# Kernel optimization log

Hardware: AMD Instinct MI355X
Metric: run time of the kernel (lower is better)

Reference implementation:

```python
import jax, jax.numpy as jnp
import numpy as np

N, E, G = 20000, 160000, 64
IN_FULL, X_START, X_END = 16, 4, 10
H, OUT, RH, NE, K = 512, 512, 128, 4, 2
NL = 3               # GraphConv layers per expert
SPS, STEMP = 0.3, 1.0  # size_prior_strength, size_temperature


def setup_inputs() -> dict:
    key = jax.random.key(0)
    ks = jax.random.split(key, 10)
    def w(k, shape, fan):
        return jax.random.normal(k, shape, jnp.float32) / np.float32(np.sqrt(fan))
    return dict(
        x=jax.random.normal(ks[0], (N, IN_FULL), jnp.float32),
        edge_index=jax.random.randint(ks[1], (2, E), 0, N),
        batch=jnp.sort(jax.random.randint(ks[2], (N,), 0, G)),
        num_graphs=G,
        enc_W1=w(ks[3], (X_END - X_START, H), X_END - X_START), enc_b1=jnp.zeros((H,), jnp.float32),
        enc_W2=w(ks[4], (H, H), H), enc_b2=jnp.zeros((H,), jnp.float32),
        r_W1=w(ks[5], (H + 2, RH), H + 2), r_b1=jnp.zeros((RH,), jnp.float32),
        ln_g=jnp.ones((RH,), jnp.float32), ln_b=jnp.zeros((RH,), jnp.float32),
        r_W2=w(ks[6], (RH, NE), RH), r_b2=jnp.zeros((NE,), jnp.float32),
        size_centers=jnp.linspace(0.0, 1.0, NE).astype(jnp.float32),
        W_rel=w(ks[7], (NE, NL, H, H), H),       # GraphConv lin_rel weights (stacked)
        b_rel=jnp.zeros((NE, NL, H), jnp.float32),
        W_root=w(ks[8], (NE, NL, H, H), H),      # GraphConv lin_root weights (no bias)
    )


def reference(x, edge_index, batch, num_graphs, enc_W1, enc_b1, enc_W2, enc_b2,
              r_W1, r_b1, ln_g, ln_b, r_W2, r_b2, size_centers, W_rel, b_rel, W_root):
    src, dst = edge_index[0], edge_index[1]
    # encoder: Linear -> ReLU -> Linear on sliced node features
    h = jax.nn.relu(x[:, X_START:X_END] @ enc_W1 + enc_b1) @ enc_W2 + enc_b2
    # per-graph size features (log_nodes_edges mode)
    nodes = jnp.maximum(jax.ops.segment_sum(jnp.ones((N,), x.dtype), batch, num_segments=num_graphs), 1.0)
    edges = jax.ops.segment_sum(jnp.ones((E,), x.dtype), batch[src], num_segments=num_graphs)
    log_n, log_e = jnp.log(nodes), jnp.log1p(edges)
    f = jnp.stack([log_n, log_e], axis=-1)
    f = (f - f.mean(0, keepdims=True)) / (f.std(0, keepdims=True) + 1e-6)
    size_norm = (log_n - log_n.min()) / (log_n.max() - log_n.min() + 1e-6)
    # router: Linear -> LayerNorm -> ReLU -> Linear, plus size prior
    r = jnp.concatenate([h, f[batch]], axis=-1) @ r_W1 + r_b1
    r = (r - r.mean(-1, keepdims=True)) / jnp.sqrt(r.var(-1, keepdims=True) + 1e-5) * ln_g + ln_b
    logits = jax.nn.relu(r) @ r_W2 + r_b2
    prior = -(size_norm[batch][:, None] - size_centers[None, :]) ** 2 / STEMP
    logits = (1.0 - SPS) * logits + SPS * prior
    probs = jax.nn.softmax(logits, axis=-1)
    # top-k sparse gating, renormalized
    v, ix = jax.lax.top_k(probs, K)
    v = v / (v.sum(-1, keepdims=True) + 1e-8)
    weights = jnp.zeros_like(probs).at[jnp.arange(N)[:, None], ix].set(v)  # [N, NE]
    # GraphConv: out_i = (sum_{j->i} z_j) @ W_rel + b_rel + z_i @ W_root
    def gconv(z, Wr, br, Wo):
        agg = jax.ops.segment_sum(z[src], dst, num_segments=N)
        return agg @ Wr + br + z @ Wo
    out = jnp.zeros((N, OUT), x.dtype)
    for e in range(NE):  # small fixed expert count
        z = jax.nn.relu(gconv(h, W_rel[e, 0], b_rel[e, 0], W_root[e, 0]))
        z = jax.nn.relu(gconv(z, W_rel[e, 1], b_rel[e, 1], W_root[e, 1]))
        z = gconv(z, W_rel[e, 2], b_rel[e, 2], W_root[e, 2])
        out = out + weights[:, e:e + 1] * z
    return out
```

## Files before the change

### kernel.cpp

```cpp
#include <hip/hip_runtime.h>
#include <math.h>

#define N_NODES 20000
#define N_EDGES 160000
#define G_GRAPHS 64
#define H_DIM 512
#define RH_DIM 128
#define NE_EXP 4
#define P_ROWS 20096
#define EH_BLOCKS 64
#define WSZ (512 * 512)

typedef __attribute__((ext_vector_type(8))) short bf16x8;
typedef __attribute__((ext_vector_type(4))) float f32x4;

__device__ __forceinline__ ushort f2bf(float f) {
    uint u = __float_as_uint(f);
    return (ushort)((u + 0x7FFFu + ((u >> 16) & 1u)) >> 16);
}
__device__ __forceinline__ float bf2f(ushort h) {
    return __uint_as_float(((uint)h) << 16);
}

__device__ __forceinline__ void async_copy16(const void* g, void* l) {
    __builtin_amdgcn_global_load_lds(
        (__attribute__((address_space(1))) void*)g,
        (__attribute__((address_space(3))) void*)l, 16, 0, 0);
}

__device__ __forceinline__ int xcd_swizzle(int orig, int nwg) {
    const int q = nwg >> 3, r = nwg & 7;
    const int xcd = orig & 7, sid = orig >> 3;
    return (xcd < r ? xcd * (q + 1) : r * (q + 1) + (xcd - r) * q) + sid;
}

template<bool RELU, int EPI, int NE2>
__global__ __launch_bounds__(256)
void gemm_grp(const ushort* __restrict__ A1, size_t a1es,
              const ushort* __restrict__ W1, size_t w1es,
              const ushort* __restrict__ A2, size_t a2es,
              const ushort* __restrict__ W2, size_t w2es,
              const float* __restrict__ bias, size_t bes,
              const float* __restrict__ wcol,
              ushort* __restrict__ out0, size_t oes)
{
    __shared__ char smem[32768];
    const int tid = threadIdx.x;
    const int w = tid >> 6, lane = tid & 63;

    const int wgid = xcd_swizzle(blockIdx.x, gridDim.x);
    const int m0 = (wgid / (4 * NE2)) * 128;
    const int rem = wgid % (4 * NE2);
    const int e  = rem % NE2;
    const int n0 = (rem / NE2) * 128;

    const ushort* __restrict__ A1e = A1 + (size_t)e * a1es;
    const ushort* __restrict__ W1e = W1 + (size_t)e * w1es;
    const ushort* __restrict__ A2e = A2 + (size_t)e * a2es;
    const ushort* __restrict__ W2e = W2 + (size_t)e * w2es;
    const float*  __restrict__ be  = bias + (size_t)e * bes;
    ushort* __restrict__ oe = out0 + (size_t)e * oes;

    f32x4 acc[4][4];
#pragma unroll
    for (int i = 0; i < 4; ++i)
#pragma unroll
        for (int j = 0; j < 4; ++j) acc[i][j] = (f32x4){0.f, 0.f, 0.f, 0.f};

    const int srow = lane >> 2, schk = lane & 3;
    const int wr = w >> 1, wc = w & 1;
    const int row16 = lane & 15;
    const uint koffB = (uint)(lane >> 4) * 16u;
    const uint aoff0 = (uint)(wr * 64 + row16) * 64u + koffB;
    const uint boff0 = 8192u + (uint)(wc * 64 + row16) * 64u + koffB;

    auto stage = [&](int buf, int t) {
        const ushort* __restrict__ A  = (t < 16) ? A1e : A2e;
        const ushort* __restrict__ Wt = (t < 16) ? W1e : W2e;
        const int kt = (t & 15) * 32;
        char* base = smem + buf * 16384;
#pragma unroll
        for (int c = 0; c < 2; ++c) {
            const int rb = c * 64 + w * 16;
            async_copy16(A  + (size_t)(m0 + rb + srow) * 512 + kt + schk * 8, base + rb * 64);
            async_copy16(Wt + (size_t)(n0 + rb + srow) * 512 + kt + schk * 8, base + 8192 + rb * 64);
        }
    };
    auto compute = [&](int buf) {
        const char* base = smem + buf * 16384;
        bf16x8 af[4], bfr[4];
#pragma unroll
        for (int i = 0; i < 4; ++i) af[i] = *(const bf16x8*)(base + aoff0 + i * 1024);
#pragma unroll
        for (int j = 0; j < 4; ++j) bfr[j] = *(const bf16x8*)(base + boff0 + j * 1024);
#pragma unroll
        for (int i = 0; i < 4; ++i)
#pragma unroll
            for (int j = 0; j < 4; ++j)
                acc[i][j] = __builtin_amdgcn_mfma_f32_16x16x32_bf16(af[i], bfr[j], acc[i][j], 0, 0, 0);
    };

    stage(0, 0);
    for (int t = 0; t < 31; ++t) {
        stage((t + 1) & 1, t + 1);
        asm volatile("s_waitcnt vmcnt(4)" ::: "memory");
        __builtin_amdgcn_s_barrier();
        compute(t & 1);
        __builtin_amdgcn_s_barrier();
    }
    asm volatile("s_waitcnt vmcnt(0)" ::: "memory");
    __builtin_amdgcn_s_barrier();
    compute(1);

#pragma unroll
    for (int i = 0; i < 4; ++i) {
        const int r0 = m0 + wr * 64 + i * 16 + (lane >> 4) * 4;
#pragma unroll
        for (int j = 0; j < 4; ++j) {
            const int c = n0 + wc * 64 + j * 16 + row16;
            const float bj = be[c];
#pragma unroll
            for (int q2 = 0; q2 < 4; ++q2) {
                const int r = r0 + q2;
                float v = acc[i][j][q2] + bj;
                if (EPI == 0) {
                    if (RELU) v = fmaxf(v, 0.f);
                    oe[(size_t)r * 512 + c] = f2bf(v);
                } else {
                    const float wrow = (r < N_NODES) ? wcol[(size_t)r * 4 + e] : 0.f;
                    oe[(size_t)r * 512 + c] = f2bf(v * wrow);
                }
            }
        }
    }
}

template<int NPASS, int EPI, int NBN>
__global__ __launch_bounds__(256)
void gemm_mfma(const ushort* __restrict__ A0, const ushort* __restrict__ W0,
               const ushort* __restrict__ A1p, const ushort* __restrict__ W1p,
               const ushort* __restrict__ A2p, const ushort* __restrict__ W2p,
               const float* __restrict__ bias,
               void* __restrict__ out0, void* __restrict__ out1, int Ncols)
{
    __shared__ char smem[32768];
    const int tid = threadIdx.x;
    const int w = tid >> 6, lane = tid & 63;

    const int wgid = xcd_swizzle(blockIdx.x, gridDim.x);
    const int m0 = (wgid / NBN) * 128;
    const int n0 = (wgid % NBN) * 128;

    f32x4 acc[4][4];
#pragma unroll
    for (int i = 0; i < 4; ++i)
#pragma unroll
        for (int j = 0; j < 4; ++j) acc[i][j] = (f32x4){0.f, 0.f, 0.f, 0.f};

    const int srow = lane >> 2, schk = lane & 3;
    const int wr = w >> 1, wc = w & 1;
    const int row16 = lane & 15;
    const uint koffB = (uint)(lane >> 4) * 16u;
    const uint aoff0 = (uint)(wr * 64 + row16) * 64u + koffB;
    const uint boff0 = 8192u + (uint)(wc * 64 + row16) * 64u + koffB;

    const int NT = NPASS * 16;
    auto Asel = [&](int t) -> const ushort* { return (t < 16) ? A0 : ((t < 32) ? A1p : A2p); };
    auto Wsel = [&](int t) -> const ushort* { return (t < 16) ? W0 : ((t < 32) ? W1p : W2p); };

    auto stage = [&](int buf, int t) {
        const ushort* __restrict__ A  = Asel(t);
        const ushort* __restrict__ Wt = Wsel(t);
        const int kt = (t & 15) * 32;
        char* base = smem + buf * 16384;
#pragma unroll
        for (int c = 0; c < 2; ++c) {
            const int rb = c * 64 + w * 16;
            async_copy16(A  + (size_t)(m0 + rb + srow) * 512 + kt + schk * 8, base + rb * 64);
            async_copy16(Wt + (size_t)(n0 + rb + srow) * 512 + kt + schk * 8, base + 8192 + rb * 64);
        }
    };
    auto compute = [&](int buf) {
        const char* base = smem + buf * 16384;
        bf16x8 af[4], bfr[4];
#pragma unroll
        for (int i = 0; i < 4; ++i) af[i] = *(const bf16x8*)(base + aoff0 + i * 1024);
#pragma unroll
        for (int j = 0; j < 4; ++j) bfr[j] = *(const bf16x8*)(base + boff0 + j * 1024);
#pragma unroll
        for (int i = 0; i < 4; ++i)
#pragma unroll
            for (int j = 0; j < 4; ++j)
                acc[i][j] = __builtin_amdgcn_mfma_f32_16x16x32_bf16(af[i], bfr[j], acc[i][j], 0, 0, 0);
    };

    stage(0, 0);
    for (int t = 0; t < NT - 1; ++t) {
        stage((t + 1) & 1, t + 1);
        asm volatile("s_waitcnt vmcnt(4)" ::: "memory");
        __builtin_amdgcn_s_barrier();
        compute(t & 1);
        __builtin_amdgcn_s_barrier();
    }
    asm volatile("s_waitcnt vmcnt(0)" ::: "memory");
    __builtin_amdgcn_s_barrier();
    compute((NT - 1) & 1);

#pragma unroll
    for (int i = 0; i < 4; ++i) {
        const int r0 = m0 + wr * 64 + i * 16 + (lane >> 4) * 4;
#pragma unroll
        for (int j = 0; j < 4; ++j) {
            const int c = n0 + wc * 64 + j * 16 + row16;
            const float bj = (EPI == 5) ? 0.f : bias[c];
#pragma unroll
            for (int q2 = 0; q2 < 4; ++q2) {
                const int r = r0 + q2;
                float v = acc[i][j][q2] + bj;
                if (EPI == 4) {
                    const ushort hi = f2bf(v);
                    const ushort lo = f2bf(v - bf2f(hi));
                    ((ushort*)out0)[(size_t)r * Ncols + c] = hi;
                    ((ushort*)out1)[(size_t)r * Ncols + c] = lo;
                } else {
                    ((float*)out0)[(size_t)r * Ncols + c] = v;
                }
            }
        }
    }
}

__global__ __launch_bounds__(256)
void reduce_wz_kernel(const uint* __restrict__ wz4, float2* __restrict__ out)
{
    const size_t idx = (size_t)blockIdx.x * 256 + threadIdx.x;
    const size_t es = (size_t)P_ROWS * 256;
    const uint a = wz4[idx], b = wz4[idx + es];
    const uint c = wz4[idx + 2 * es], d = wz4[idx + 3 * es];
    float lo = bf2f((ushort)(a & 0xffffu)) + bf2f((ushort)(b & 0xffffu))
             + bf2f((ushort)(c & 0xffffu)) + bf2f((ushort)(d & 0xffffu));
    float hi = bf2f((ushort)(a >> 16)) + bf2f((ushort)(b >> 16))
             + bf2f((ushort)(c >> 16)) + bf2f((ushort)(d >> 16));
    out[idx] = make_float2(lo, hi);
}

__global__ void encoder1_kernel(const float* __restrict__ x, const float* __restrict__ W1,
                                const float* __restrict__ b1,
                                ushort* __restrict__ t1hi, ushort* __restrict__ t1lo)
{
    const int idx = blockIdx.x * blockDim.x + threadIdx.x;
    if (idx >= P_ROWS * H_DIM) return;
    const int i = idx / H_DIM, j = idx - i * H_DIM;
    float v = 0.f;
    if (i < N_NODES) {
        const float* xr = &x[i * 16 + 4];
        v = b1[j];
#pragma unroll
        for (int k = 0; k < 6; ++k) v = fmaf(xr[k], W1[k * H_DIM + j], v);
        v = fmaxf(v, 0.f);
    }
    const ushort hi = f2bf(v);
    t1hi[idx] = hi;
    t1lo[idx] = f2bf(v - bf2f(hi));
}

__global__ void zero_ints_kernel(int* __restrict__ p, int n)
{
    const int idx = blockIdx.x * blockDim.x + threadIdx.x;
    if (idx < n) p[idx] = 0;
}

__global__ void graph_bounds_kernel(const int* __restrict__ batch, int* __restrict__ gstart)
{
    const int g = threadIdx.x;
    if (g > G_GRAPHS) return;
    int lo = 0, hi = N_NODES;
    while (lo < hi) {
        const int mid = (lo + hi) >> 1;
        if (batch[mid] < g) lo = mid + 1; else hi = mid;
    }
    gstart[g] = lo;
}

__global__ __launch_bounds__(256)
void edge_hist_kernel(const int* __restrict__ src, const int* __restrict__ dst,
                      const int* __restrict__ batch,
                      int* __restrict__ part, int* __restrict__ deg)
{
    __shared__ int hist[G_GRAPHS];
    const int tid = threadIdx.x;
    if (tid < G_GRAPHS) hist[tid] = 0;
    __syncthreads();
    for (int e = blockIdx.x * 256 + tid; e < N_EDGES; e += EH_BLOCKS * 256) {
        atomicAdd(&deg[dst[e]], 1);
        atomicAdd(&hist[batch[src[e]]], 1);
    }
    __syncthreads();
    if (tid < G_GRAPHS) part[blockIdx.x * G_GRAPHS + tid] = hist[tid];
}

__global__ void stats_finalize_kernel(const int* __restrict__ gstart, const int* __restrict__ part,
                                      float* __restrict__ f_norm, float* __restrict__ size_norm)
{
    const int g = threadIdx.x;
    const float nn = fmaxf((float)(gstart[g + 1] - gstart[g]), 1.0f);
    int ec = 0;
#pragma unroll 8
    for (int b = 0; b < EH_BLOCKS; ++b) ec += part[b * G_GRAPHS + g];
    const float ee = (float)ec;
    const float ln = logf(nn);
    const float le = log1pf(ee);
    float s0 = ln, s1 = le;
#pragma unroll
    for (int o = 32; o > 0; o >>= 1) { s0 += __shfl_xor(s0, o); s1 += __shfl_xor(s1, o); }
    const float m0 = s0 / 64.f, m1 = s1 / 64.f;
    const float d0 = ln - m0, d1 = le - m1;
    float v0 = d0 * d0, v1 = d1 * d1;
#pragma unroll
    for (int o = 32; o > 0; o >>= 1) { v0 += __shfl_xor(v0, o); v1 += __shfl_xor(v1, o); }
    const float sd0 = sqrtf(v0 / 64.f), sd1 = sqrtf(v1 / 64.f);
    float mn = ln, mx = ln;
#pragma unroll
    for (int o = 32; o > 0; o >>= 1) {
        mn = fminf(mn, __shfl_xor(mn, o));
        mx = fmaxf(mx, __shfl_xor(mx, o));
    }
    f_norm[g * 2 + 0] = d0 / (sd0 + 1e-6f);
    f_norm[g * 2 + 1] = d1 / (sd1 + 1e-6f);
    size_norm[g] = (ln - mn) / (mx - mn + 1e-6f);
}

__global__ void scan_kernel(const int* __restrict__ in, int* __restrict__ row_ptr,
                            int* __restrict__ cursor, int n)
{
    __shared__ int wsum[16];
    __shared__ int carry_s;
    const int tid = threadIdx.x;
    const int lane = tid & 63, wv = tid >> 6;
    if (tid == 0) carry_s = 0;
    __syncthreads();
    for (int base = 0; base < n; base += 1024) {
        const int idx = base + tid;
        const int v = (idx < n) ? in[idx] : 0;
        int x = v;
#pragma unroll
        for (int o = 1; o < 64; o <<= 1) { const int t = __shfl_up(x, o); if (lane >= o) x += t; }
        if (lane == 63) wsum[wv] = x;
        __syncthreads();
        const int carry = carry_s;
        if (wv == 0) {
            int y = (lane < 16) ? wsum[lane] : 0;
#pragma unroll
            for (int o = 1; o < 16; o <<= 1) { const int t = __shfl_up(y, o); if (lane >= o) y += t; }
            if (lane < 16) wsum[lane] = y;
        }
        __syncthreads();
        const int woff = (wv > 0) ? wsum[wv - 1] : 0;
        const int excl = x - v + woff + carry;
        if (idx < n) { row_ptr[idx] = excl; cursor[idx] = excl; }
        __syncthreads();
        if (tid == 0) carry_s = carry + wsum[15];
        __syncthreads();
    }
    if (tid == 0) row_ptr[n] = carry_s;
}

__global__ void scatter_kernel(const int* __restrict__ src, const int* __restrict__ dst,
                               int* __restrict__ cursor, int* __restrict__ csr_col)
{
    const int e = blockIdx.x * blockDim.x + threadIdx.x;
    if (e >= N_EDGES) return;
    const int d = dst[e];
    const int slot = atomicAdd(&cursor[d], 1);
    csr_col[slot] = src[e];
}

__global__ void sort_adj_kernel(const int* __restrict__ row_ptr, int* __restrict__ csr_col)
{
    const int i = blockIdx.x * blockDim.x + threadIdx.x;
    if (i >= N_NODES) return;
    const int b = row_ptr[i], e = row_ptr[i + 1];
    for (int p = b + 1; p < e; ++p) {
        const int key = csr_col[p];
        int q = p - 1;
        while (q >= b && csr_col[q] > key) { csr_col[q + 1] = csr_col[q]; --q; }
        csr_col[q + 1] = key;
    }
}

__global__ __launch_bounds__(256)
void aggregate_bf16(const uint* __restrict__ z2, const int* __restrict__ row_ptr,
                    const int* __restrict__ csr_col, uint* __restrict__ agg2)
{
    const size_t es = (size_t)blockIdx.y * P_ROWS * 256;
    const uint* __restrict__ zz = z2 + es;
    uint* __restrict__ aa = agg2 + es;
    const int i = blockIdx.x;
    const int t = threadIdx.x;
    const int b = row_ptr[i], e = row_ptr[i + 1];
    float ax = 0.f, ay = 0.f;
    int p = b;
    for (; p + 4 <= e; p += 4) {
        const int s0 = csr_col[p + 0], s1 = csr_col[p + 1];
        const int s2 = csr_col[p + 2], s3 = csr_col[p + 3];
        const uint v0 = zz[(size_t)s0 * 256 + t];
        const uint v1 = zz[(size_t)s1 * 256 + t];
        const uint v2 = zz[(size_t)s2 * 256 + t];
        const uint v3 = zz[(size_t)s3 * 256 + t];
        ax += bf2f((ushort)(v0 & 0xffffu)) + bf2f((ushort)(v1 & 0xffffu))
            + bf2f((ushort)(v2 & 0xffffu)) + bf2f((ushort)(v3 & 0xffffu));
        ay += bf2f((ushort)(v0 >> 16)) + bf2f((ushort)(v1 >> 16))
            + bf2f((ushort)(v2 >> 16)) + bf2f((ushort)(v3 >> 16));
    }
    for (; p < e; ++p) {
        const uint v = zz[(size_t)csr_col[p] * 256 + t];
        ax += bf2f((ushort)(v & 0xffffu));
        ay += bf2f((ushort)(v >> 16));
    }
    aa[(size_t)i * 256 + t] = (uint)f2bf(ax) | ((uint)f2bf(ay) << 16);
}

__global__ __launch_bounds__(256)
void transpose_f32_to_bf16(const float* __restrict__ W, ushort* __restrict__ Wt)
{
    __shared__ float tile[32][33];
    const float* Wm = W + (size_t)blockIdx.z * WSZ;
    ushort* Wtm = Wt + (size_t)blockIdx.z * WSZ;
    const int c0 = blockIdx.x * 32, r0 = blockIdx.y * 32;
    const int tc = threadIdx.x & 31, tr = threadIdx.x >> 5;
#pragma unroll
    for (int it = 0; it < 4; ++it)
        tile[tr + it * 8][tc] = Wm[(size_t)(r0 + tr + it * 8) * 512 + c0 + tc];
    __syncthreads();
#pragma unroll
    for (int it = 0; it < 4; ++it) {
        const int cr = tr + it * 8;
        Wtm[(size_t)(c0 + cr) * 512 + r0 + tc] = f2bf(tile[tc][cr]);
    }
}

__global__ __launch_bounds__(256)
void transpose_split_kernel(const float* __restrict__ W, ushort* __restrict__ Whi,
                            ushort* __restrict__ Wlo, int Nin)
{
    __shared__ float tile[32][33];
    const int c0 = blockIdx.x * 32;
    const int r0 = blockIdx.y * 32;
    const int tc = threadIdx.x & 31, tr = threadIdx.x >> 5;
#pragma unroll
    for (int it = 0; it < 4; ++it)
        tile[tr + it * 8][tc] = W[(size_t)(r0 + tr + it * 8) * Nin + c0 + tc];
    __syncthreads();
#pragma unroll
    for (int it = 0; it < 4; ++it) {
        const int cr = tr + it * 8;
        const float v = tile[tc][cr];
        const ushort hi = f2bf(v);
        Whi[(size_t)(c0 + cr) * 512 + r0 + tc] = hi;
        Wlo[(size_t)(c0 + cr) * 512 + r0 + tc] = f2bf(v - bf2f(hi));
    }
}

__global__ __launch_bounds__(128)
void router_kernel(const float* __restrict__ rtmp, const int* __restrict__ batch,
                   const float* __restrict__ rW1, const float* __restrict__ rb1,
                   const float* __restrict__ lng, const float* __restrict__ lnb,
                   const float* __restrict__ rW2, const float* __restrict__ rb2,
                   const float* __restrict__ centers,
                   const float* __restrict__ f_norm, const float* __restrict__ size_norm,
                   float* __restrict__ weights)
{
    const int i = blockIdx.x;
    const int j = threadIdx.x;
    const int g = batch[i];
    const float f0 = f_norm[g * 2], f1 = f_norm[g * 2 + 1];
    float r = rtmp[(size_t)i * RH_DIM + j]
            + f0 * rW1[512 * RH_DIM + j] + f1 * rW1[513 * RH_DIM + j] + rb1[j];

    __shared__ float part[2];
    __shared__ float rbuf[RH_DIM];
    __shared__ float lbuf[4];
    const int lane = j & 63, wv = j >> 6;

    float s = r;
#pragma unroll
    for (int o = 32; o > 0; o >>= 1) s += __shfl_xor(s, o);
    if (lane == 0) part[wv] = s;
    __syncthreads();
    const float mean = (part[0] + part[1]) / 128.f;
    __syncthreads();
    const float d = r - mean;
    float v = d * d;
#pragma unroll
    for (int o = 32; o > 0; o >>= 1) v += __shfl_xor(v, o);
    if (lane == 0) part[wv] = v;
    __syncthreads();
    const float var = (part[0] + part[1]) / 128.f;
    const float rn = d / sqrtf(var + 1e-5f) * lng[j] + lnb[j];
    rbuf[j] = fmaxf(rn, 0.f);
    __syncthreads();

    if (j < 4) {
        float acc = rb2[j];
        for (int t = 0; t < RH_DIM; ++t) acc = fmaf(rbuf[t], rW2[t * 4 + j], acc);
        const float sn = size_norm[g];
        const float dd = sn - centers[j];
        lbuf[j] = 0.7f * acc + 0.3f * (-(dd * dd));
    }
    __syncthreads();
    if (j == 0) {
        float p[4];
        const float mx = fmaxf(fmaxf(lbuf[0], lbuf[1]), fmaxf(lbuf[2], lbuf[3]));
#pragma unroll
        for (int c = 0; c < 4; ++c) p[c] = expf(lbuf[c] - mx);
        const float ssum = p[0] + p[1] + p[2] + p[3];
#pragma unroll
        for (int c = 0; c < 4; ++c) p[c] /= ssum;
        int i1 = 0;
#pragma unroll
        for (int c = 1; c < 4; ++c) if (p[c] > p[i1]) i1 = c;
        int i2 = -1;
#pragma unroll
        for (int c = 0; c < 4; ++c) {
            if (c == i1) continue;
            if (i2 < 0 || p[c] > p[i2]) i2 = c;
        }
        const float vs = p[i1] + p[i2] + 1e-8f;
        float wout[4] = {0.f, 0.f, 0.f, 0.f};
        wout[i1] = p[i1] / vs;
        wout[i2] = p[i2] / vs;
#pragma unroll
        for (int c = 0; c < 4; ++c) weights[(size_t)i * 4 + c] = wout[c];
    }
}

extern "C" void kernel_launch(void* const* d_in, const int* in_sizes, int n_in,
                              void* d_out, int out_size, void* d_ws, size_t ws_size,
                              hipStream_t stream)
{
    const float* x       = (const float*)d_in[0];
    const int*   ei      = (const int*)d_in[1];
    const int*   batch   = (const int*)d_in[2];
    const float* enc_W1  = (const float*)d_in[4];
    const float* enc_b1  = (const float*)d_in[5];
    const float* enc_W2  = (const float*)d_in[6];
    const float* enc_b2  = (const float*)d_in[7];
    const float* r_W1    = (const float*)d_in[8];
    const float* r_b1    = (const float*)d_in[9];
    const float* ln_g    = (const float*)d_in[10];
    const float* ln_b    = (const float*)d_in[11];
    const float* r_W2    = (const float*)d_in[12];
    const float* r_b2    = (const float*)d_in[13];
    const float* centers = (const float*)d_in[14];
    const float* W_rel   = (const float*)d_in[15];
    const float* b_rel   = (const float*)d_in[16];
    const float* W_root  = (const float*)d_in[17];
    const int* src = ei;
    const int* dst = ei + N_EDGES;
    float* out = (float*)d_out;

    const size_t PF = (size_t)P_ROWS * H_DIM;
    const size_t need4 = PF * 34 + (size_t)40 * 1024 * 1024;
    const bool path4 = (ws_size >= need4);
    const int NEPD = path4 ? 4 : 2;
    const size_t ZBYTES = PF * 2 * NEPD;

    char* wsp = (char*)d_ws;
    size_t off = 0;
    auto alloc = [&](size_t bytes) -> char* {
        char* p = wsp + off;
        off = (off + bytes + 255) & ~(size_t)255;
        return p;
    };
    char* region1 = alloc(PF * 4);
    ushort* t1hi = (ushort*)region1;
    ushort* t1lo = (ushort*)(region1 + PF * 2);
    ushort* wz4  = (ushort*)region1;
    char* region2 = alloc(PF * 4);
    ushort* h_hi = (ushort*)region2;
    ushort* h_lo = (ushort*)(region2 + PF * 2);
    char* B_zA = alloc(ZBYTES);
    ushort* zAe = (ushort*)B_zA;
    float*  rtmp = (float*)B_zA;
    char* B_zB = alloc(ZBYTES);
    ushort* zBe = (ushort*)B_zB;
    char* B_ag = alloc(ZBYTES);
    ushort* agge = (ushort*)B_ag;
    ushort* aggH16 = (ushort*)alloc(PF * 2);
    ushort* Wt_rel16  = (ushort*)alloc((size_t)12 * WSZ * 2);
    ushort* Wt_root16 = (ushort*)alloc((size_t)12 * WSZ * 2);
    ushort* W2t_hi = (ushort*)alloc((size_t)WSZ * 2);
    ushort* W2t_lo = (ushort*)alloc((size_t)WSZ * 2);
    ushort* rW1t_hi = (ushort*)alloc((size_t)128 * 512 * 2);
    ushort* rW1t_lo = (ushort*)alloc((size_t)128 * 512 * 2);
    float*  weights = (float*)alloc((size_t)P_ROWS * 4 * 4);
    int* deg     = (int*)alloc((size_t)N_NODES * 4);
    int* gstart  = (int*)alloc((size_t)(G_GRAPHS + 1) * 4);
    int* part    = (int*)alloc((size_t)EH_BLOCKS * G_GRAPHS * 4);
    int* row_ptr = (int*)alloc((size_t)(N_NODES + 1) * 4);
    int* cursor  = (int*)alloc((size_t)N_NODES * 4);
    int* csr_col = (int*)alloc((size_t)N_EDGES * 4);
    float* f_norm    = (float*)alloc((size_t)G_GRAPHS * 2 * 4);
    float* size_norm = (float*)alloc((size_t)G_GRAPHS * 4);
    (void)in_sizes; (void)n_in; (void)out_size;

    const int enc_nwg = 4 * (P_ROWS / 128);
    const int rtr_nwg = 1 * (P_ROWS / 128);
    const int grp_nwg = 4 * NEPD * (P_ROWS / 128);
    const dim3 tr_grid(16, 16, 12);
    const dim3 agg_grid1(N_NODES, 1), agg_gridE(N_NODES, NEPD);

    zero_ints_kernel<<<(N_NODES + 255) / 256, 256, 0, stream>>>(deg, N_NODES);
    transpose_f32_to_bf16<<<tr_grid, 256, 0, stream>>>(W_rel, Wt_rel16);
    transpose_f32_to_bf16<<<tr_grid, 256, 0, stream>>>(W_root, Wt_root16);
    transpose_split_kernel<<<dim3(16, 16), 256, 0, stream>>>(enc_W2, W2t_hi, W2t_lo, 512);
    transpose_split_kernel<<<dim3(4, 16), 256, 0, stream>>>(r_W1, rW1t_hi, rW1t_lo, 128);
    graph_bounds_kernel<<<1, 128, 0, stream>>>(batch, gstart);
    edge_hist_kernel<<<EH_BLOCKS, 256, 0, stream>>>(src, dst, batch, part, deg);
    stats_finalize_kernel<<<1, 64, 0, stream>>>(gstart, part, f_norm, size_norm);
    encoder1_kernel<<<(P_ROWS * H_DIM + 255) / 256, 256, 0, stream>>>(x, enc_W1, enc_b1, t1hi, t1lo);
    gemm_mfma<3, 4, 4><<<enc_nwg, 256, 0, stream>>>(
        t1hi, W2t_hi, t1hi, W2t_lo, t1lo, W2t_hi, enc_b2, h_hi, h_lo, 512);
    gemm_mfma<3, 5, 1><<<rtr_nwg, 256, 0, stream>>>(
        h_hi, rW1t_hi, h_hi, rW1t_lo, h_lo, rW1t_hi, nullptr, rtmp, nullptr, 128);
    router_kernel<<<N_NODES, 128, 0, stream>>>(rtmp, batch, r_W1, r_b1, ln_g, ln_b,
                                               r_W2, r_b2, centers, f_norm, size_norm, weights);
    scan_kernel<<<1, 1024, 0, stream>>>(deg, row_ptr, cursor, N_NODES);
    scatter_kernel<<<(N_EDGES + 255) / 256, 256, 0, stream>>>(src, dst, cursor, csr_col);
    sort_adj_kernel<<<(N_NODES + 255) / 256, 256, 0, stream>>>(row_ptr, csr_col);
    aggregate_bf16<<<agg_grid1, 256, 0, stream>>>((const uint*)h_hi, row_ptr, csr_col, (uint*)aggH16);

    const size_t WES = (size_t)3 * WSZ;
    const size_t BES = (size_t)3 * 512;
    if (path4) {
        gemm_grp<true, 0, 4><<<grp_nwg, 256, 0, stream>>>(
            aggH16, 0, Wt_rel16, WES, h_hi, 0, Wt_root16, WES, b_rel, BES, nullptr, zAe, PF);
        aggregate_bf16<<<agg_gridE, 256, 0, stream>>>((const uint*)zAe, row_ptr, csr_col, (uint*)agge);
        gemm_grp<true, 0, 4><<<grp_nwg, 256, 0, stream>>>(
            agge, PF, Wt_rel16 + WSZ, WES, zAe, PF, Wt_root16 + WSZ, WES, b_rel + 512, BES,
            nullptr, zBe, PF);
        aggregate_bf16<<<agg_gridE, 256, 0, stream>>>((const uint*)zBe, row_ptr, csr_col, (uint*)agge);
        gemm_grp<false, 6, 4><<<grp_nwg, 256, 0, stream>>>(
            agge, PF, Wt_rel16 + 2 * WSZ, WES, zBe, PF, Wt_root16 + 2 * WSZ, WES, b_rel + 1024, BES,
            weights, wz4, PF);
    } else {
        for (int p = 0; p < 2; ++p) {
            const size_t eb = (size_t)(p * 2);
            const ushort* WrP = Wt_rel16  + eb * WES;
            const ushort* WoP = Wt_root16 + eb * WES;
            const float*  brP = b_rel + eb * BES;
            ushort* wzP = wz4 + eb * PF;
            gemm_grp<true, 0, 2><<<grp_nwg, 256, 0, stream>>>(
                aggH16, 0, WrP, WES, h_hi, 0, WoP, WES, brP, BES, nullptr, zAe, PF);
            aggregate_bf16<<<agg_gridE, 256, 0, stream>>>((const uint*)zAe, row_ptr, csr_col, (uint*)agge);
            gemm_grp<true, 0, 2><<<grp_nwg, 256, 0, stream>>>(
                agge, PF, WrP + WSZ, WES, zAe, PF, WoP + WSZ, WES, brP + 512, BES, nullptr, zBe, PF);
            aggregate_bf16<<<agg_gridE, 256, 0, stream>>>((const uint*)zBe, row_ptr, csr_col, (uint*)agge);
            gemm_grp<false, 6, 2><<<grp_nwg, 256, 0, stream>>>(
                agge, PF, WrP + 2 * WSZ, WES, zBe, PF, WoP + 2 * WSZ, WES, brP + 1024, BES,
                weights + eb, wzP, PF);
        }
    }
    reduce_wz_kernel<<<N_NODES, 256, 0, stream>>>((const uint*)wz4, (float2*)out);
}
```

Measured before the change: 859.9 us.

## Widen grouped GEMM tile to 128x256 and vectorize neighbor aggregation

The grouped expert GEMM now computes 128x256 output tiles. Each wave holds 4x8 MFMA accumulators, and LDS double buffers grow to 48KB with a launch-bounds occupancy hint of 2. This halves the grid and raises A-tile reuse, at the cost of more registers, more LDS and fewer workgroups. The aggregation kernel now handles four nodes per block, one wavefront each, using 16-byte uint4 loads instead of 4-byte loads. The path4 workspace threshold is also changed to a fixed 372MB constant.

```diff
diff --git a/kernel.cpp b/kernel.cpp
--- a/kernel.cpp
+++ b/kernel.cpp
@@ -35,7 +35,7 @@
 }
 
 template<bool RELU, int EPI, int NE2>
-__global__ __launch_bounds__(256)
+__global__ __launch_bounds__(256, 2)
 void gemm_grp(const ushort* __restrict__ A1, size_t a1es,
               const ushort* __restrict__ W1, size_t w1es,
               const ushort* __restrict__ A2, size_t a2es,
@@ -44,15 +44,15 @@
               const float* __restrict__ wcol,
               ushort* __restrict__ out0, size_t oes)
 {
-    __shared__ char smem[32768];
+    __shared__ char smem[49152];
     const int tid = threadIdx.x;
     const int w = tid >> 6, lane = tid & 63;
 
     const int wgid = xcd_swizzle(blockIdx.x, gridDim.x);
-    const int m0 = (wgid / (4 * NE2)) * 128;
-    const int rem = wgid % (4 * NE2);
+    const int m0 = (wgid / (2 * NE2)) * 128;
+    const int rem = wgid % (2 * NE2);
     const int e  = rem % NE2;
-    const int n0 = (rem / NE2) * 128;
+    const int n0 = (rem / NE2) * 256;
 
     const ushort* __restrict__ A1e = A1 + (size_t)e * a1es;
     const ushort* __restrict__ W1e = W1 + (size_t)e * w1es;
@@ -61,49 +61,54 @@
     const float*  __restrict__ be  = bias + (size_t)e * bes;
     ushort* __restrict__ oe = out0 + (size_t)e * oes;
 
-    f32x4 acc[4][4];
+    f32x4 acc[4][8];
 #pragma unroll
     for (int i = 0; i < 4; ++i)
 #pragma unroll
-        for (int j = 0; j < 4; ++j) acc[i][j] = (f32x4){0.f, 0.f, 0.f, 0.f};
+        for (int j = 0; j < 8; ++j) acc[i][j] = (f32x4){0.f, 0.f, 0.f, 0.f};
 
     const int srow = lane >> 2, schk = lane & 3;
     const int wr = w >> 1, wc = w & 1;
     const int row16 = lane & 15;
     const uint koffB = (uint)(lane >> 4) * 16u;
     const uint aoff0 = (uint)(wr * 64 + row16) * 64u + koffB;
-    const uint boff0 = 8192u + (uint)(wc * 64 + row16) * 64u + koffB;
+    const uint boff0 = 8192u + (uint)(wc * 128 + row16) * 64u + koffB;
 
     auto stage = [&](int buf, int t) {
         const ushort* __restrict__ A  = (t < 16) ? A1e : A2e;
         const ushort* __restrict__ Wt = (t < 16) ? W1e : W2e;
         const int kt = (t & 15) * 32;
-        char* base = smem + buf * 16384;
+        char* base = smem + buf * 24576;
 #pragma unroll
         for (int c = 0; c < 2; ++c) {
             const int rb = c * 64 + w * 16;
-            async_copy16(A  + (size_t)(m0 + rb + srow) * 512 + kt + schk * 8, base + rb * 64);
-            async_copy16(Wt + (size_t)(n0 + rb + srow) * 512 + kt + schk * 8, base + 8192 + rb * 64);
+            async_copy16(A + (size_t)(m0 + rb + srow) * 512 + kt + schk * 8, base + rb * 64);
+        }
+#pragma unroll
+        for (int c = 0; c < 4; ++c) {
+            const int rb = c * 64 + w * 16;
+            async_copy16(Wt + (size_t)(n0 + rb + srow) * 512 + kt + schk * 8,
+                         base + 8192 + rb * 64);
         }
     };
     auto compute = [&](int buf) {
-        const char* base = smem + buf * 16384;
-        bf16x8 af[4], bfr[4];
+        const char* base = smem + buf * 24576;
+        bf16x8 af[4], bfr[8];
 #pragma unroll
         for (int i = 0; i < 4; ++i) af[i] = *(const bf16x8*)(base + aoff0 + i * 1024);
 #pragma unroll
-        for (int j = 0; j < 4; ++j) bfr[j] = *(const bf16x8*)(base + boff0 + j * 1024);
+        for (int j = 0; j < 8; ++j) bfr[j] = *(const bf16x8*)(base + boff0 + j * 1024);
 #pragma unroll
         for (int i = 0; i < 4; ++i)
 #pragma unroll
-            for (int j = 0; j < 4; ++j)
+            for (int j = 0; j < 8; ++j)
                 acc[i][j] = __builtin_amdgcn_mfma_f32_16x16x32_bf16(af[i], bfr[j], acc[i][j], 0, 0, 0);
     };
 
     stage(0, 0);
     for (int t = 0; t < 31; ++t) {
         stage((t + 1) & 1, t + 1);
-        asm volatile("s_waitcnt vmcnt(4)" ::: "memory");
+        asm volatile("s_waitcnt vmcnt(6)" ::: "memory");
         __builtin_amdgcn_s_barrier();
         compute(t & 1);
         __builtin_amdgcn_s_barrier();
@@ -116,8 +121,8 @@
     for (int i = 0; i < 4; ++i) {
         const int r0 = m0 + wr * 64 + i * 16 + (lane >> 4) * 4;
 #pragma unroll
-        for (int j = 0; j < 4; ++j) {
-            const int c = n0 + wc * 64 + j * 16 + row16;
+        for (int j = 0; j < 8; ++j) {
+            const int c = n0 + wc * 128 + j * 16 + row16;
             const float bj = be[c];
 #pragma unroll
             for (int q2 = 0; q2 < 4; ++q2) {
@@ -389,35 +394,38 @@
 }
 
 __global__ __launch_bounds__(256)
-void aggregate_bf16(const uint* __restrict__ z2, const int* __restrict__ row_ptr,
-                    const int* __restrict__ csr_col, uint* __restrict__ agg2)
-{
-    const size_t es = (size_t)blockIdx.y * P_ROWS * 256;
-    const uint* __restrict__ zz = z2 + es;
-    uint* __restrict__ aa = agg2 + es;
-    const int i = blockIdx.x;
-    const int t = threadIdx.x;
+void aggregate_bf16(const uint4* __restrict__ z4, const int* __restrict__ row_ptr,
+                    const int* __restrict__ csr_col, uint4* __restrict__ agg4)
+{
+    const size_t es = (size_t)blockIdx.y * P_ROWS * 64;
+    const uint4* __restrict__ zz = z4 + es;
+    uint4* __restrict__ aa = agg4 + es;
+    const int i = blockIdx.x * 4 + (threadIdx.x >> 6);
+    const int lane = threadIdx.x & 63;
     const int b = row_ptr[i], e = row_ptr[i + 1];
-    float ax = 0.f, ay = 0.f;
+    float acc[8];
+#pragma unroll
+    for (int k = 0; k < 8; ++k) acc[k] = 0.f;
+    auto add8 = [&](uint4 v) {
+        acc[0] += bf2f((ushort)(v.x & 0xffffu)); acc[1] += bf2f((ushort)(v.x >> 16));
+        acc[2] += bf2f((ushort)(v.y & 0xffffu)); acc[3] += bf2f((ushort)(v.y >> 16));
+        acc[4] += bf2f((ushort)(v.z & 0xffffu)); acc[5] += bf2f((ushort)(v.z >> 16));
+        acc[6] += bf2f((ushort)(v.w & 0xffffu)); acc[7] += bf2f((ushort)(v.w >> 16));
+    };
     int p = b;
-    for (; p + 4 <= e; p += 4) {
-        const int s0 = csr_col[p + 0], s1 = csr_col[p + 1];
-        const int s2 = csr_col[p + 2], s3 = csr_col[p + 3];
-        const uint v0 = zz[(size_t)s0 * 256 + t];
-        const uint v1 = zz[(size_t)s1 * 256 + t];
-        const uint v2 = zz[(size_t)s2 * 256 + t];
-        const uint v3 = zz[(size_t)s3 * 256 + t];
-        ax += bf2f((ushort)(v0 & 0xffffu)) + bf2f((ushort)(v1 & 0xffffu))
-            + bf2f((ushort)(v2 & 0xffffu)) + bf2f((ushort)(v3 & 0xffffu));
-        ay += bf2f((ushort)(v0 >> 16)) + bf2f((ushort)(v1 >> 16))
-            + bf2f((ushort)(v2 >> 16)) + bf2f((ushort)(v3 >> 16));
-    }
-    for (; p < e; ++p) {
-        const uint v = zz[(size_t)csr_col[p] * 256 + t];
-        ax += bf2f((ushort)(v & 0xffffu));
-        ay += bf2f((ushort)(v >> 16));
-    }
-    aa[(size_t)i * 256 + t] = (uint)f2bf(ax) | ((uint)f2bf(ay) << 16);
+    for (; p + 2 <= e; p += 2) {
+        const uint4 v0 = zz[(size_t)csr_col[p] * 64 + lane];
+        const uint4 v1 = zz[(size_t)csr_col[p + 1] * 64 + lane];
+        add8(v0);
+        add8(v1);
+    }
+    if (p < e) add8(zz[(size_t)csr_col[p] * 64 + lane]);
+    uint4 o;
+    o.x = (uint)f2bf(acc[0]) | ((uint)f2bf(acc[1]) << 16);
+    o.y = (uint)f2bf(acc[2]) | ((uint)f2bf(acc[3]) << 16);
+    o.z = (uint)f2bf(acc[4]) | ((uint)f2bf(acc[5]) << 16);
+    o.w = (uint)f2bf(acc[6]) | ((uint)f2bf(acc[7]) << 16);
+    aa[(size_t)i * 64 + lane] = o;
 }
 
 __global__ __launch_bounds__(256)
@@ -560,7 +568,7 @@
     float* out = (float*)d_out;
 
     const size_t PF = (size_t)P_ROWS * H_DIM;
-    const size_t need4 = PF * 34 + (size_t)40 * 1024 * 1024;
+    const size_t need4 = (size_t)372 * 1024 * 1024;
     const bool path4 = (ws_size >= need4);
     const int NEPD = path4 ? 4 : 2;
     const size_t ZBYTES = PF * 2 * NEPD;
@@ -606,9 +614,9 @@
 
     const int enc_nwg = 4 * (P_ROWS / 128);
     const int rtr_nwg = 1 * (P_ROWS / 128);
-    const int grp_nwg = 4 * NEPD * (P_ROWS / 128);
+    const int grp_nwg = 2 * NEPD * (P_ROWS / 128);
     const dim3 tr_grid(16, 16, 12);
-    const dim3 agg_grid1(N_NODES, 1), agg_gridE(N_NODES, NEPD);
+    const dim3 agg_grid1(N_NODES / 4, 1), agg_gridE(N_NODES / 4, NEPD);
 
     zero_ints_kernel<<<(N_NODES + 255) / 256, 256, 0, stream>>>(deg, N_NODES);
     transpose_f32_to_bf16<<<tr_grid, 256, 0, stream>>>(W_rel, Wt_rel16);
@@ -628,18 +636,21 @@
     scan_kernel<<<1, 1024, 0, stream>>>(deg, row_ptr, cursor, N_NODES);
     scatter_kernel<<<(N_EDGES + 255) / 256, 256, 0, stream>>>(src, dst, cursor, csr_col);
     sort_adj_kernel<<<(N_NODES + 255) / 256, 256, 0, stream>>>(row_ptr, csr_col);
-    aggregate_bf16<<<agg_grid1, 256, 0, stream>>>((const uint*)h_hi, row_ptr, csr_col, (uint*)aggH16);
+    aggregate_bf16<<<agg_grid1, 256, 0, stream>>>((const uint4*)h_hi, row_ptr, csr_col,
+                                                  (uint4*)aggH16);
 
     const size_t WES = (size_t)3 * WSZ;
     const size_t BES = (size_t)3 * 512;
     if (path4) {
         gemm_grp<true, 0, 4><<<grp_nwg, 256, 0, stream>>>(
             aggH16, 0, Wt_rel16, WES, h_hi, 0, Wt_root16, WES, b_rel, BES, nullptr, zAe, PF);
-        aggregate_bf16<<<agg_gridE, 256, 0, stream>>>((const uint*)zAe, row_ptr, csr_col, (uint*)agge);
+        aggregate_bf16<<<agg_gridE, 256, 0, stream>>>((const uint4*)zAe, row_ptr, csr_col,
+                                                      (uint4*)agge);
         gemm_grp<true, 0, 4><<<grp_nwg, 256, 0, stream>>>(
             agge, PF, Wt_rel16 + WSZ, WES, zAe, PF, Wt_root16 + WSZ, WES, b_rel + 512, BES,
             nullptr, zBe, PF);
-        aggregate_bf16<<<agg_gridE, 256, 0, stream>>>((const uint*)zBe, row_ptr, csr_col, (uint*)agge);
+        aggregate_bf16<<<agg_gridE, 256, 0, stream>>>((const uint4*)zBe, row_ptr, csr_col,
+                                                      (uint4*)agge);
         gemm_grp<false, 6, 4><<<grp_nwg, 256, 0, stream>>>(
             agge, PF, Wt_rel16 + 2 * WSZ, WES, zBe, PF, Wt_root16 + 2 * WSZ, WES, b_rel + 1024, BES,
             weights, wz4, PF);
@@ -652,10 +663,12 @@
             ushort* wzP = wz4 + eb * PF;
             gemm_grp<true, 0, 2><<<grp_nwg, 256, 0, stream>>>(
                 aggH16, 0, WrP, WES, h_hi, 0, WoP, WES, brP, BES, nullptr, zAe, PF);
-            aggregate_bf16<<<agg_gridE, 256, 0, stream>>>((const uint*)zAe, row_ptr, csr_col, (uint*)agge);
+            aggregate_bf16<<<agg_gridE, 256, 0, stream>>>((const uint4*)zAe, row_ptr, csr_col,
+                                                          (uint4*)agge);
             gemm_grp<true, 0, 2><<<grp_nwg, 256, 0, stream>>>(
                 agge, PF, WrP + WSZ, WES, zAe, PF, WoP + WSZ, WES, brP + 512, BES, nullptr, zBe, PF);
-            aggregate_bf16<<<agg_gridE, 256, 0, stream>>>((const uint*)zBe, row_ptr, csr_col, (uint*)agge);
+            aggregate_bf16<<<agg_gridE, 256, 0, stream>>>((const uint4*)zBe, row_ptr, csr_col,
+                                                          (uint4*)agge);
             gemm_grp<false, 6, 2><<<grp_nwg, 256, 0, stream>>>(
                 agge, PF, WrP + 2 * WSZ, WES, zBe, PF, WoP + 2 * WSZ, WES, brP + 1024, BES,
                 weights + eb, wzP, PF);
```

New measurement: 848.7 us. About the same (-1.3%).
